# Kernel tuning notes

Measured on AMD Instinct MI355X. Metric: run time of the kernel, lower is better.

The kernel has to match this reference:

```python
import jax, jax.numpy as jnp
import numpy as np

J = 17
MIN_TORSO_H = 10.0
MAX_RANGE = 5.0
EPS = 1e-6
LN_EPS = 1e-5
LS, RS, LH, RH = 5, 6, 11, 12  # COCO shoulder/hip indices


def _mid(pl, pr, cl, cr):
    # conf-weighted midpoint: both valid -> mean, one valid -> that one, none -> 0
    wl = (cl > 0).astype(pl.dtype)[:, None]
    wr = (cr > 0).astype(pr.dtype)[:, None]
    s = wl * pl + wr * pr
    w = wl + wr
    return s / jnp.maximum(w, 1.0)


def torso_centric(kp):
    pos = kp[..., :2]          # [B, J, 2]
    conf = kp[..., 2:3]        # [B, J, 1]
    sc = conf[:, [LS, RS], 0]  # [B, 2]
    hc = conf[:, [LH, RH], 0]
    use_torso = ((sc > 0).sum(1) >= 1) & ((hc > 0).sum(1) >= 1)  # [B]
    sm = _mid(pos[:, LS], pos[:, RS], sc[:, 0], sc[:, 1])  # [B, 2]
    hm = _mid(pos[:, LH], pos[:, RH], hc[:, 0], hc[:, 1])
    sm = jnp.where(use_torso[:, None], sm, 0.0)
    hm = jnp.where(use_torso[:, None], hm, 0.0)
    center = (sm + hm) * 0.5                                   # [B, 2]
    height = jnp.linalg.norm(sm - hm, axis=1, keepdims=True)   # [B, 1]
    valid = use_torso & (height[:, 0] >= MIN_TORSO_H)
    torso_np = jnp.clip((pos - center[:, None, :]) / (height[:, None, :] + EPS),
                        -MAX_RANGE, MAX_RANGE)
    # bbox fallback (bbox computed from keypoints)
    mn = pos.min(axis=1, keepdims=True)
    mx = pos.max(axis=1, keepdims=True)
    bbox_np = jnp.clip((pos - mn) / (mx - mn + EPS), -MAX_RANGE, MAX_RANGE)
    norm_pos = jnp.where(valid[:, None, None], torso_np, bbox_np)
    return jnp.concatenate([norm_pos, conf], axis=-1)


def _ln(x, g, b):
    m = x.mean(-1, keepdims=True)
    v = ((x - m) ** 2).mean(-1, keepdims=True)
    return (x - m) / jnp.sqrt(v + LN_EPS) * g + b


def setup_inputs() -> dict:
    key = jax.random.key(0)
    ks = jax.random.split(key, 24)
    B = 32768

    def mk_kp(k0, k1, k2):
        pos = jax.random.uniform(k0, (B, J, 2)) * 512.0
        conf = jax.random.uniform(k1, (B, J, 1))
        conf = jnp.where(jax.random.uniform(k2, (B, J, 1)) < 0.2, 0.0, conf)
        return jnp.concatenate([pos, conf], -1)

    inp = {
        'keypoints': mk_kp(ks[0], ks[1], ks[2]),
        'prev_keypoints': mk_kp(ks[3], ks[4], ks[5]),
        'joint_emb': jax.random.normal(ks[6], (J, 16)) * 0.05,
        'pos_W': jax.random.normal(ks[7], (2, 16)) * 0.05, 'pos_b': jnp.zeros((16,)),
        'vel_W': jax.random.normal(ks[8], (2, 8)) * 0.05, 'vel_b': jnp.zeros((8,)),
        'angvel_W': jax.random.normal(ks[9], (3, 8)) * 0.05, 'angvel_b': jnp.zeros((8,)),
        'rel_W': jax.random.normal(ks[10], (2, 8)) * 0.05, 'rel_b': jnp.zeros((8,)),
        'conf_W': jax.random.normal(ks[11], (1, 4)) * 0.05, 'conf_b': jnp.zeros((4,)),
        'p1_W': jax.random.normal(ks[12], (60, 128)) * 0.05, 'p1_b': jnp.zeros((128,)),
        'ln1_g': jnp.ones((128,)), 'ln1_b': jnp.zeros((128,)),
        'p2_W': jax.random.normal(ks[13], (128, 64)) * 0.05, 'p2_b': jnp.zeros((64,)),
        'ln2_g': jnp.ones((64,)), 'ln2_b': jnp.zeros((64,)),
    }
    return inp


def reference(keypoints, prev_keypoints, joint_emb,
              pos_W, pos_b, vel_W, vel_b, angvel_W, angvel_b,
              rel_W, rel_b, conf_W, conf_b,
              p1_W, p1_b, ln1_g, ln1_b, p2_W, p2_b, ln2_g, ln2_b):
    B = keypoints.shape[0]
    kp = torso_centric(keypoints)
    pkp = torso_centric(prev_keypoints)
    pos = kp[..., :2]
    conf = kp[..., 2:3]

    type_emb = jnp.broadcast_to(joint_emb[None], (B, J, 16))
    pos_emb = pos @ pos_W + pos_b                               # [B,J,16]
    vel = pos - pkp[..., :2]
    vel_emb = vel @ vel_W + vel_b                               # [B,J,8]
    # use_angles=False -> angular velocities are zeros through the encoder
    angvel_emb = jnp.broadcast_to(angvel_b[None, None], (B, J, 8))
    # relative position to torso center (mean of shoulder/hip joints)
    torso_center = pos[:, jnp.array([LS, RS, LH, RH])].mean(axis=1, keepdims=True)
    rel_emb = (pos - torso_center) @ rel_W + rel_b              # [B,J,8]
    conf_emb = conf @ conf_W + conf_b                           # [B,J,4]

    feats = jnp.concatenate([type_emb, pos_emb, vel_emb, angvel_emb,
                             rel_emb, conf_emb], axis=-1)       # [B,J,60]
    h = _ln(feats @ p1_W + p1_b, ln1_g, ln1_b)
    h = jax.nn.relu(h)                                          # dropout is identity (eval)
    out = _ln(h @ p2_W + p2_b, ln2_g, ln2_b)                    # [B,J,64]
    return out
```

## Files before the change

kernel.cpp:

```cpp
#include <hip/hip_runtime.h>
#include <hip/hip_bf16.h>

#define NJ 17
#define ROWS 32
#define TPB 256
#define TOKPB (ROWS * NJ)

#define LSJ 5
#define RSJ 6
#define LHJ 11
#define RHJ 12

#define WSU_A1   4096
#define WSU_PRM  6144

#define SH_G1P  4096
#define SH_B1P  4160
#define SH_LN2  4224
#define SH_U32  4416

typedef __attribute__((ext_vector_type(8))) short bf16x8;
typedef __attribute__((ext_vector_type(8))) _Float16 f16x8;
typedef __attribute__((ext_vector_type(2))) _Float16 f16x2;
typedef __attribute__((ext_vector_type(4))) float f32x4;
typedef __attribute__((ext_vector_type(4))) unsigned int u32x4;

__device__ __forceinline__ unsigned short f2hu(float x) {
    _Float16 h = (_Float16)x;
    return __builtin_bit_cast(unsigned short, h);
}
__device__ __forceinline__ f16x2 cvt2h(float lo, float hi) {
    return __builtin_bit_cast(f16x2, __builtin_amdgcn_cvt_pkrtz(lo, hi));
}

__device__ __forceinline__ float row16_sum(float s) {
    int t;
    t = __builtin_amdgcn_update_dpp(0, __builtin_bit_cast(int, s), 0x121, 0xf, 0xf, true);
    s += __builtin_bit_cast(float, t);
    t = __builtin_amdgcn_update_dpp(0, __builtin_bit_cast(int, s), 0x122, 0xf, 0xf, true);
    s += __builtin_bit_cast(float, t);
    t = __builtin_amdgcn_update_dpp(0, __builtin_bit_cast(int, s), 0x124, 0xf, 0xf, true);
    s += __builtin_bit_cast(float, t);
    t = __builtin_amdgcn_update_dpp(0, __builtin_bit_cast(int, s), 0x128, 0xf, 0xf, true);
    s += __builtin_bit_cast(float, t);
    return s;
}

__device__ __forceinline__ void norm_row(const float* __restrict__ r,
                                         float* __restrict__ ox,
                                         float* __restrict__ oy) {
    float sc0 = r[LSJ*3+2], sc1 = r[RSJ*3+2];
    float hc0 = r[LHJ*3+2], hc1 = r[RHJ*3+2];
    bool ut = ((sc0 > 0.f) || (sc1 > 0.f)) && ((hc0 > 0.f) || (hc1 > 0.f));

    float wl = sc0 > 0.f ? 1.f : 0.f;
    float wr = sc1 > 0.f ? 1.f : 0.f;
    float ws = fmaxf(wl + wr, 1.f);
    float smx = (wl * r[LSJ*3+0] + wr * r[RSJ*3+0]) / ws;
    float smy = (wl * r[LSJ*3+1] + wr * r[RSJ*3+1]) / ws;

    wl = hc0 > 0.f ? 1.f : 0.f;
    wr = hc1 > 0.f ? 1.f : 0.f;
    ws = fmaxf(wl + wr, 1.f);
    float hmx = (wl * r[LHJ*3+0] + wr * r[RHJ*3+0]) / ws;
    float hmy = (wl * r[LHJ*3+1] + wr * r[RHJ*3+1]) / ws;

    if (!ut) { smx = 0.f; smy = 0.f; hmx = 0.f; hmy = 0.f; }

    float cx = (smx + hmx) * 0.5f;
    float cy = (smy + hmy) * 0.5f;
    float dx = smx - hmx, dy = smy - hmy;
    float hh = sqrtf(dx * dx + dy * dy);
    bool valid = ut && (hh >= 10.0f);

    float mnx = r[0], mxx = r[0], mny = r[1], mxy = r[1];
    #pragma unroll
    for (int j = 1; j < NJ; ++j) {
        float x = r[j*3], y = r[j*3+1];
        mnx = fminf(mnx, x); mxx = fmaxf(mxx, x);
        mny = fminf(mny, y); mxy = fmaxf(mxy, y);
    }

    float ih  = 1.f / (hh + 1e-6f);
    float ibx = 1.f / (mxx - mnx + 1e-6f);
    float iby = 1.f / (mxy - mny + 1e-6f);

    #pragma unroll
    for (int j = 0; j < NJ; ++j) {
        float x = r[j*3], y = r[j*3+1];
        float tx = (x - cx) * ih, ty = (y - cy) * ih;
        float bx = (x - mnx) * ibx, by = (y - mny) * iby;
        float nx = valid ? tx : bx;
        float ny = valid ? ty : by;
        ox[j] = fminf(fmaxf(nx, -5.f), 5.f);
        oy[j] = fminf(fmaxf(ny, -5.f), 5.f);
    }
}

__global__ __launch_bounds__(256) void setup_kernel(
    const float* __restrict__ emb,
    const float* __restrict__ posW, const float* __restrict__ posB,
    const float* __restrict__ velW, const float* __restrict__ velB,
    const float* __restrict__ angB,
    const float* __restrict__ relW, const float* __restrict__ relB,
    const float* __restrict__ confW, const float* __restrict__ confB,
    const float* __restrict__ P1, const float* __restrict__ p1b,
    const float* __restrict__ g1, const float* __restrict__ b1,
    const float* __restrict__ W2, const float* __restrict__ p2b,
    const float* __restrict__ g2, const float* __restrict__ b2,
    unsigned int* __restrict__ ws)
{
    __shared__ float sPA[7][128];
    __shared__ float sBase[128];
    __shared__ float sK0[17][128];
    const int tid = threadIdx.x;

    if (tid < 128) {
        const int n = tid;
        float pa0 = 0.f, pa1 = 0.f;
        #pragma unroll
        for (int i = 0; i < 16; ++i) {
            float w = P1[(16 + i) * 128 + n];
            pa0 += posW[i] * w; pa1 += posW[16 + i] * w;
        }
        float pv0 = 0.f, pv1 = 0.f;
        #pragma unroll
        for (int i = 0; i < 8; ++i) {
            float w = P1[(32 + i) * 128 + n];
            pv0 += velW[i] * w; pv1 += velW[8 + i] * w;
        }
        float pr0 = 0.f, pr1 = 0.f;
        #pragma unroll
        for (int i = 0; i < 8; ++i) {
            float w = P1[(48 + i) * 128 + n];
            pr0 += relW[i] * w; pr1 += relW[8 + i] * w;
        }
        float pc = 0.f;
        #pragma unroll
        for (int i = 0; i < 4; ++i) pc += confW[i] * P1[(56 + i) * 128 + n];

        float base = p1b[n];
        #pragma unroll
        for (int i = 0; i < 16; ++i) base += posB[i]  * P1[(16 + i) * 128 + n];
        #pragma unroll
        for (int i = 0; i < 8; ++i)  base += velB[i]  * P1[(32 + i) * 128 + n];
        #pragma unroll
        for (int i = 0; i < 8; ++i)  base += angB[i]  * P1[(40 + i) * 128 + n];
        #pragma unroll
        for (int i = 0; i < 8; ++i)  base += relB[i]  * P1[(48 + i) * 128 + n];
        #pragma unroll
        for (int i = 0; i < 4; ++i)  base += confB[i] * P1[(56 + i) * 128 + n];

        sPA[0][n] = pa0; sPA[1][n] = pa1;
        sPA[2][n] = pv0; sPA[3][n] = pv1;
        sPA[4][n] = pr0; sPA[5][n] = pr1;
        sPA[6][n] = pc;  sBase[n] = base;
    } else {
        const int t = tid - 128;
        const int n = t & 63;
        const int gp = (t >> 6) * 2;
        const unsigned xm = (unsigned)(n & 15) << 4;
        #pragma unroll
        for (int dg = 0; dg < 2; ++dg) {
            const int gg = gp + dg;
            #pragma unroll
            for (int ks = 0; ks < 4; ++ks) {
                unsigned int pk[4];
                #pragma unroll
                for (int ep = 0; ep < 4; ++ep) {
                    int e0 = 2 * ep, e1 = 2 * ep + 1;
                    int c0 = 4 * gg + (e0 & 3) + 16 * (2 * ks + (e0 >> 2));
                    int c1 = 4 * gg + (e1 & 3) + 16 * (2 * ks + (e1 >> 2));
                    unsigned lo = f2hu(W2[c0 * 64 + n]);
                    unsigned hi = f2hu(W2[c1 * 64 + n]);
                    pk[ep] = lo | (hi << 16);
                }
                unsigned byte = (unsigned)n * 256u + ((unsigned)((ks * 4 + gg) * 16) ^ xm);
                *(u32x4*)&ws[byte >> 2] = (u32x4){pk[0], pk[1], pk[2], pk[3]};
            }
        }
    }

    if (tid < 32) {
        const int gg = tid >> 3, nt1 = tid & 7;
        const int c0 = 4 * gg + 16 * nt1;
        ws[WSU_PRM + tid * 2 + 0]      = (unsigned)f2hu(g1[c0+0]) | ((unsigned)f2hu(g1[c0+1]) << 16);
        ws[WSU_PRM + tid * 2 + 1]      = (unsigned)f2hu(g1[c0+2]) | ((unsigned)f2hu(g1[c0+3]) << 16);
        ws[WSU_PRM + 64 + tid * 2 + 0] = (unsigned)f2hu(b1[c0+0]) | ((unsigned)f2hu(b1[c0+1]) << 16);
        ws[WSU_PRM + 64 + tid * 2 + 1] = (unsigned)f2hu(b1[c0+2]) | ((unsigned)f2hu(b1[c0+3]) << 16);
    } else if (tid >= 64 && tid < 256) {
        const int i = tid - 64;
        float v = (i < 64) ? g2[i] : (i < 128 ? b2[i - 64] : p2b[i - 128]);
        ws[WSU_PRM + 128 + i] = __builtin_bit_cast(unsigned, v);
    }
    __syncthreads();

    for (int e = tid; e < NJ * 128; e += 256) {
        int j = e >> 7, n = e & 127;
        float v = sBase[n];
        #pragma unroll
        for (int t = 0; t < 16; ++t) v += emb[j * 16 + t] * P1[t * 128 + n];
        sK0[j][n] = v;
    }
    __syncthreads();

    for (int i = tid; i < 512; i += 256) {
        const int nt1 = i >> 6, ln = i & 63, gg = ln >> 4, tl2 = ln & 15;
        const int ch = tl2 + 16 * nt1;
        float w[8];
        #pragma unroll
        for (int e = 0; e < 8; ++e) w[e] = 0.f;
        if (gg == 0) {
            #pragma unroll
            for (int e = 0; e < 7; ++e) w[e] = sPA[e][ch];
            w[7] = sK0[0][ch];
        } else if (gg == 1) {
            #pragma unroll
            for (int e = 0; e < 8; ++e) w[e] = sK0[e + 1][ch];
        } else if (gg == 2) {
            #pragma unroll
            for (int e = 0; e < 8; ++e) w[e] = sK0[e + 9][ch];
        }
        unsigned u[4];
        #pragma unroll
        for (int p = 0; p < 4; ++p) {
            unsigned short lo = f2hu(w[2*p]);
            unsigned short hi = f2hu(w[2*p+1]);
            u[p] = (unsigned)lo | ((unsigned)hi << 16);
        }
        *(u32x4*)&ws[WSU_A1 + i * 4] = (u32x4){u[0], u[1], u[2], u[3]};
    }
}

__global__ __launch_bounds__(TPB, 2)
void jfe_kernel(
    const float* __restrict__ kp, const float* __restrict__ pkp,
    const unsigned int* __restrict__ ws,
    float* __restrict__ out, int B)
{
    __shared__ __align__(16) unsigned int sWS[SH_U32];
    __shared__ __align__(16) unsigned int sA1[2176];
    __shared__ __align__(16) float4 sPk[TOKPB];
    __shared__ __align__(8)  float2 sQ[TOKPB];
    __shared__ float2 sTc[ROWS];

    const int tid  = threadIdx.x;
    const int lane = tid & 63;
    const int wv   = tid >> 6;
    const int g    = lane >> 4;
    const int tl   = lane & 15;

    const int row0  = blockIdx.x * ROWS;
    const int nrows = min(ROWS, B - row0);
    const long long tok0 = (long long)blockIdx.x * TOKPB;
    const long long ntok = (long long)B * NJ;

    for (int c = tid; c < 1024; c += TPB)
        *(u32x4*)&sWS[c * 4] = *(const u32x4*)&ws[c * 4];
    for (int c = tid; c < 512; c += TPB)
        *(u32x4*)&sA1[c * 4] = *(const u32x4*)&ws[WSU_A1 + c * 4];
    if (tid < 80)
        *(u32x4*)&sWS[SH_G1P + tid * 4] = *(const u32x4*)&ws[WSU_PRM + tid * 4];

    if (tl < 16 && g == 0) {
        const int task  = wv * 16 + tl;
        const int frame = task >> 5;
        const int row   = task & 31;
        if (row < nrows) {
            float ox[NJ], oy[NJ];
            if (frame == 0) {
                const float* rp = kp + (long long)(row0 + row) * 51;
                norm_row(rp, ox, oy);
                #pragma unroll
                for (int j = 0; j < NJ; ++j)
                    sPk[row * NJ + j] = make_float4(ox[j], oy[j], rp[j * 3 + 2], 0.f);
                sTc[row] = make_float2(
                    0.25f * (ox[LSJ] + ox[RSJ] + ox[LHJ] + ox[RHJ]),
                    0.25f * (oy[LSJ] + oy[RSJ] + oy[LHJ] + oy[RHJ]));
            } else {
                norm_row(pkp + (long long)(row0 + row) * 51, ox, oy);
                #pragma unroll
                for (int j = 0; j < NJ; ++j)
                    sQ[row * NJ + j] = make_float2(ox[j], oy[j]);
            }
        }
    }
    __syncthreads();

    f16x8 a1f[8];
    #pragma unroll
    for (int nt1 = 0; nt1 < 8; ++nt1)
        a1f[nt1] = __builtin_bit_cast(f16x8,
            *(const u32x4*)&sA1[(nt1 * 64 + lane) * 4]);

    f16x2 g1h[8][2], b1h[8][2];
    #pragma unroll
    for (int nt1 = 0; nt1 < 8; ++nt1) {
        g1h[nt1][0] = __builtin_bit_cast(f16x2, sWS[SH_G1P + (g * 8 + nt1) * 2 + 0]);
        g1h[nt1][1] = __builtin_bit_cast(f16x2, sWS[SH_G1P + (g * 8 + nt1) * 2 + 1]);
        b1h[nt1][0] = __builtin_bit_cast(f16x2, sWS[SH_B1P + (g * 8 + nt1) * 2 + 0]);
        b1h[nt1][1] = __builtin_bit_cast(f16x2, sWS[SH_B1P + (g * 8 + nt1) * 2 + 1]);
    }
    float g2v[4], b2v[4], p2v[4];
    #pragma unroll
    for (int nt = 0; nt < 4; ++nt) {
        g2v[nt] = __builtin_bit_cast(float, sWS[SH_LN2 +   0 + 4 * tl + nt]);
        b2v[nt] = __builtin_bit_cast(float, sWS[SH_LN2 +  64 + 4 * tl + nt]);
        p2v[nt] = __builtin_bit_cast(float, sWS[SH_LN2 + 128 + nt * 16 + tl]);
    }
    __syncthreads();

    float* const sXp = (float*)sA1 + wv * 544 + g * 136;

    const bool full = (nrows == ROWS);
    const int ntiles = (nrows * NJ + 15) >> 4;
    const unsigned xm = (unsigned)tl << 4;

    #pragma unroll 1
    for (int t = wv; t < ntiles; t += 4) {
        const int tbase = t * 16;
        const int tok = tbase + tl;
        const int r = (tok * 3856) >> 16;
        const int j = tok - r * NJ;

        const float4 pk = sPk[tok];
        const float2 qv = sQ[tok];
        const float2 tc = sTc[r];
        const float px = pk.x, py = pk.y, cf = pk.z;
        const float vx = px - qv.x, vy = py - qv.y;
        const float rx = px - tc.x, ry = py - tc.y;

        f16x8 bf;
        {
            const int base7 = g * 8 - 7;
            #pragma unroll
            for (int e = 0; e < 8; ++e) {
                float oh = ((base7 + e) == j) ? 1.f : 0.f;
                float val;
                if (e == 0) val = (g == 0) ? px : oh;
                else if (e == 1) val = (g == 0) ? py : oh;
                else if (e == 2) val = (g == 0) ? vx : oh;
                else if (e == 3) val = (g == 0) ? vy : oh;
                else if (e == 4) val = (g == 0) ? rx : oh;
                else if (e == 5) val = (g == 0) ? ry : oh;
                else if (e == 6) val = (g == 0) ? cf : oh;
                else val = oh;
                bf[e] = (_Float16)val;
            }
        }

        f32x4 acc1[8];
        #pragma unroll
        for (int nt1 = 0; nt1 < 8; ++nt1)
            acc1[nt1] = __builtin_amdgcn_mfma_f32_16x16x32_f16(
                a1f[nt1], bf, (f32x4){0.f, 0.f, 0.f, 0.f}, 0, 0, 0);

        float s, ss;
        {
            float t0[8], t1[8];
            #pragma unroll
            for (int n1 = 0; n1 < 8; ++n1) {
                float a0 = acc1[n1][0], a1 = acc1[n1][1];
                float a2 = acc1[n1][2], a3 = acc1[n1][3];
                t0[n1] = (a0 + a1) + (a2 + a3);
                t1[n1] = (a0 * a0 + a1 * a1) + (a2 * a2 + a3 * a3);
            }
            s  = ((t0[0] + t0[1]) + (t0[2] + t0[3])) + ((t0[4] + t0[5]) + (t0[6] + t0[7]));
            ss = ((t1[0] + t1[1]) + (t1[2] + t1[3])) + ((t1[4] + t1[5]) + (t1[6] + t1[7]));
        }
        s += __shfl_xor(s, 16); ss += __shfl_xor(ss, 16);
        s += __shfl_xor(s, 32); ss += __shfl_xor(ss, 32);
        const float mu  = s * (1.f / 128.f);
        const float inv = rsqrtf(ss * (1.f / 128.f) - mu * mu + 1e-5f);

        const f16x2 im2 = cvt2h(inv, inv);
        const f16x2 nm2 = cvt2h(-mu * inv, -mu * inv);
        const f16x2 zero2 = (f16x2)(_Float16)0.f;
        u32x4 afu[4];
        #pragma unroll
        for (int nt1 = 0; nt1 < 8; ++nt1) {
            const int ks = nt1 >> 1, sl = 2 * (nt1 & 1);
            f16x2 a01 = cvt2h(acc1[nt1][0], acc1[nt1][1]);
            f16x2 a23 = cvt2h(acc1[nt1][2], acc1[nt1][3]);
            f16x2 s01 = g1h[nt1][0] * im2;
            f16x2 s23 = g1h[nt1][1] * im2;
            f16x2 c01 = g1h[nt1][0] * nm2 + b1h[nt1][0];
            f16x2 c23 = g1h[nt1][1] * nm2 + b1h[nt1][1];
            f16x2 t01 = __builtin_elementwise_max(a01 * s01 + c01, zero2);
            f16x2 t23 = __builtin_elementwise_max(a23 * s23 + c23, zero2);
            afu[ks][sl + 0] = __builtin_bit_cast(unsigned, t01);
            afu[ks][sl + 1] = __builtin_bit_cast(unsigned, t23);
        }

        f32x4 acc2[4];
        #pragma unroll
        for (int nt = 0; nt < 4; ++nt)
            acc2[nt] = (f32x4){p2v[nt], p2v[nt], p2v[nt], p2v[nt]};
        #pragma unroll
        for (int ks = 0; ks < 4; ++ks) {
            const unsigned so = ((unsigned)((ks * 4 + g) * 16) ^ xm) >> 2;
            const f16x8 afk = __builtin_bit_cast(f16x8, afu[ks]);
            #pragma unroll
            for (int nt = 0; nt < 4; ++nt) {
                const unsigned idx = (unsigned)(nt * 16 + tl) * 64u + so;
                f16x8 bw = __builtin_bit_cast(f16x8, *(const u32x4*)&sWS[idx]);
                acc2[nt] = __builtin_amdgcn_mfma_f32_16x16x32_f16(afk, bw, acc2[nt], 0, 0, 0);
            }
        }

        float vm[4], vi[4];
        #pragma unroll
        for (int q = 0; q < 4; ++q) {
            float a0 = acc2[0][q], a1 = acc2[1][q], a2 = acc2[2][q], a3 = acc2[3][q];
            float s2 = row16_sum((a0 + a1) + (a2 + a3));
            float q2 = row16_sum((a0 * a0 + a1 * a1) + (a2 * a2 + a3 * a3));
            vm[q] = s2 * (1.f / 64.f);
            vi[q] = rsqrtf(q2 * (1.f / 64.f) - vm[q] * vm[q] + 1e-5f);
        }
        float* const obase = out + (((long long)(tok0 + tbase) + g * 4) << 6) + 4 * tl;

#define WRQ(q, rr) { \
        float* d = sXp + (rr) * 68; \
        d[ 0 + tl] = (acc2[0][q] - vm[q]) * vi[q]; \
        d[16 + tl] = (acc2[1][q] - vm[q]) * vi[q]; \
        d[32 + tl] = (acc2[2][q] - vm[q]) * vi[q]; \
        d[48 + tl] = (acc2[3][q] - vm[q]) * vi[q]; }
#define RDQ(q, rr) { \
        f32x4 w = *(const f32x4*)&sXp[(rr) * 68 + 4 * tl]; \
        f32x4 v; \
        v[0] = w[0] * g2v[0] + b2v[0]; v[1] = w[1] * g2v[1] + b2v[1]; \
        v[2] = w[2] * g2v[2] + b2v[2]; v[3] = w[3] * g2v[3] + b2v[3]; \
        *(f32x4*)(obase + (q) * 64) = v; }
#define RDQG(q, rr) { \
        if (tok0 + tbase + g * 4 + (q) < ntok) RDQ(q, rr) }

        if (full) {
            WRQ(0, 0); WRQ(1, 1); RDQ(0, 0);
            WRQ(2, 0); RDQ(1, 1);
            WRQ(3, 1); RDQ(2, 0); RDQ(3, 1);
        } else {
            WRQ(0, 0); WRQ(1, 1); RDQG(0, 0);
            WRQ(2, 0); RDQG(1, 1);
            WRQ(3, 1); RDQG(2, 0); RDQG(3, 1);
        }
#undef WRQ
#undef RDQ
#undef RDQG
    }
}

extern "C" void kernel_launch(void* const* d_in, const int* in_sizes, int n_in,
                              void* d_out, int out_size, void* d_ws, size_t ws_size,
                              hipStream_t stream) {
    const float* kp    = (const float*)d_in[0];
    const float* pkp   = (const float*)d_in[1];
    const float* emb   = (const float*)d_in[2];
    const float* posW  = (const float*)d_in[3];
    const float* posB  = (const float*)d_in[4];
    const float* velW  = (const float*)d_in[5];
    const float* velB  = (const float*)d_in[6];
    const float* angB  = (const float*)d_in[8];
    const float* relW  = (const float*)d_in[9];
    const float* relB  = (const float*)d_in[10];
    const float* confW = (const float*)d_in[11];
    const float* confB = (const float*)d_in[12];
    const float* P1    = (const float*)d_in[13];
    const float* p1b   = (const float*)d_in[14];
    const float* g1    = (const float*)d_in[15];
    const float* b1    = (const float*)d_in[16];
    const float* W2    = (const float*)d_in[17];
    const float* p2b   = (const float*)d_in[18];
    const float* g2    = (const float*)d_in[19];
    const float* b2    = (const float*)d_in[20];
    float* out = (float*)d_out;
    unsigned int* ws = (unsigned int*)d_ws;

    int B = in_sizes[0] / (NJ * 3);

    setup_kernel<<<1, 256, 0, stream>>>(
        emb, posW, posB, velW, velB, angB, relW, relB, confW, confB,
        P1, p1b, g1, b1, W2, p2b, g2, b2, ws);

    int nblocks = (B + ROWS - 1) / ROWS;
    jfe_kernel<<<nblocks, TPB, 0, stream>>>(kp, pkp, ws, out, B);
}
```

Baseline: 59.61 us.

## Software-pipeline tile loop: issue next tile's first GEMM before current epilogue

Splits the per-tile body into a front stage (input gather plus first MFMA layer) and a back stage (LayerNorm, second MFMA, output). The loop is restructured with double-buffered accumulators so the next tile's first-layer MFMAs are issued before the current tile's back stage, letting matrix work overlap with the ALU, shuffle and store work. It also folds the final LN subtraction into an FMA. Holding two sets of accumulators raises register pressure under a 2-waves launch bound, which may cause spills. The first front_tile runs unguarded even when a wave has no tile.

```diff
diff --git a/kernel.cpp b/kernel.cpp
--- a/kernel.cpp
+++ b/kernel.cpp
@@ -230,6 +230,148 @@
         }
         *(u32x4*)&ws[WSU_A1 + i * 4] = (u32x4){u[0], u[1], u[2], u[3]};
     }
+}
+
+__device__ __forceinline__ void front_tile(
+    const int tbase, const int tl, const int g,
+    const float4* __restrict__ sPk, const float2* __restrict__ sQ,
+    const float2* __restrict__ sTc,
+    const f16x8 (&a1f)[8], f32x4 (&acc1)[8])
+{
+    const int tok = tbase + tl;
+    const int r = (tok * 3856) >> 16;
+    const int j = tok - r * NJ;
+
+    const float4 pk = sPk[tok];
+    const float2 qv = sQ[tok];
+    const float2 tc = sTc[r];
+    const float px = pk.x, py = pk.y, cf = pk.z;
+    const float vx = px - qv.x, vy = py - qv.y;
+    const float rx = px - tc.x, ry = py - tc.y;
+
+    f16x8 bf;
+    const int base7 = g * 8 - 7;
+    #pragma unroll
+    for (int e = 0; e < 8; ++e) {
+        float oh = ((base7 + e) == j) ? 1.f : 0.f;
+        float val;
+        if (e == 0) val = (g == 0) ? px : oh;
+        else if (e == 1) val = (g == 0) ? py : oh;
+        else if (e == 2) val = (g == 0) ? vx : oh;
+        else if (e == 3) val = (g == 0) ? vy : oh;
+        else if (e == 4) val = (g == 0) ? rx : oh;
+        else if (e == 5) val = (g == 0) ? ry : oh;
+        else if (e == 6) val = (g == 0) ? cf : oh;
+        else val = oh;
+        bf[e] = (_Float16)val;
+    }
+
+    #pragma unroll
+    for (int nt1 = 0; nt1 < 8; ++nt1)
+        acc1[nt1] = __builtin_amdgcn_mfma_f32_16x16x32_f16(
+            a1f[nt1], bf, (f32x4){0.f, 0.f, 0.f, 0.f}, 0, 0, 0);
+}
+
+__device__ __forceinline__ void back_tile(
+    const int tbase, const int tl, const int g, const unsigned xm,
+    const long long tok0, const long long ntok, const bool full,
+    const unsigned int* __restrict__ sWS, float* __restrict__ sXp,
+    const f16x2 (&g1h)[8][2], const f16x2 (&b1h)[8][2],
+    const float (&g2v)[4], const float (&b2v)[4], const float (&p2v)[4],
+    const f32x4 (&acc1)[8], float* __restrict__ out)
+{
+    float s, ss;
+    {
+        float t0[8], t1[8];
+        #pragma unroll
+        for (int n1 = 0; n1 < 8; ++n1) {
+            float a0 = acc1[n1][0], a1 = acc1[n1][1];
+            float a2 = acc1[n1][2], a3 = acc1[n1][3];
+            t0[n1] = (a0 + a1) + (a2 + a3);
+            t1[n1] = (a0 * a0 + a1 * a1) + (a2 * a2 + a3 * a3);
+        }
+        s  = ((t0[0] + t0[1]) + (t0[2] + t0[3])) + ((t0[4] + t0[5]) + (t0[6] + t0[7]));
+        ss = ((t1[0] + t1[1]) + (t1[2] + t1[3])) + ((t1[4] + t1[5]) + (t1[6] + t1[7]));
+    }
+    s += __shfl_xor(s, 16); ss += __shfl_xor(ss, 16);
+    s += __shfl_xor(s, 32); ss += __shfl_xor(ss, 32);
+    const float mu  = s * (1.f / 128.f);
+    const float inv = rsqrtf(ss * (1.f / 128.f) - mu * mu + 1e-5f);
+
+    const f16x2 im2 = cvt2h(inv, inv);
+    const f16x2 nm2 = cvt2h(-mu * inv, -mu * inv);
+    const f16x2 zero2 = (f16x2)(_Float16)0.f;
+    u32x4 afu[4];
+    #pragma unroll
+    for (int nt1 = 0; nt1 < 8; ++nt1) {
+        const int ks = nt1 >> 1, sl = 2 * (nt1 & 1);
+        f16x2 a01 = cvt2h(acc1[nt1][0], acc1[nt1][1]);
+        f16x2 a23 = cvt2h(acc1[nt1][2], acc1[nt1][3]);
+        f16x2 s01 = g1h[nt1][0] * im2;
+        f16x2 s23 = g1h[nt1][1] * im2;
+        f16x2 c01 = g1h[nt1][0] * nm2 + b1h[nt1][0];
+        f16x2 c23 = g1h[nt1][1] * nm2 + b1h[nt1][1];
+        f16x2 t01 = __builtin_elementwise_max(a01 * s01 + c01, zero2);
+        f16x2 t23 = __builtin_elementwise_max(a23 * s23 + c23, zero2);
+        afu[ks][sl + 0] = __builtin_bit_cast(unsigned, t01);
+        afu[ks][sl + 1] = __builtin_bit_cast(unsigned, t23);
+    }
+
+    f32x4 acc2[4];
+    #pragma unroll
+    for (int nt = 0; nt < 4; ++nt)
+        acc2[nt] = (f32x4){p2v[nt], p2v[nt], p2v[nt], p2v[nt]};
+    #pragma unroll
+    for (int ks = 0; ks < 4; ++ks) {
+        const unsigned so = ((unsigned)((ks * 4 + g) * 16) ^ xm) >> 2;
+        const f16x8 afk = __builtin_bit_cast(f16x8, afu[ks]);
+        #pragma unroll
+        for (int nt = 0; nt < 4; ++nt) {
+            const unsigned idx = (unsigned)(nt * 16 + tl) * 64u + so;
+            f16x8 bw = __builtin_bit_cast(f16x8, *(const u32x4*)&sWS[idx]);
+            acc2[nt] = __builtin_amdgcn_mfma_f32_16x16x32_f16(afk, bw, acc2[nt], 0, 0, 0);
+        }
+    }
+
+    float vi[4], nvi[4];
+    #pragma unroll
+    for (int q = 0; q < 4; ++q) {
+        float a0 = acc2[0][q], a1 = acc2[1][q], a2 = acc2[2][q], a3 = acc2[3][q];
+        float s2 = row16_sum((a0 + a1) + (a2 + a3));
+        float q2 = row16_sum((a0 * a0 + a1 * a1) + (a2 * a2 + a3 * a3));
+        float m = s2 * (1.f / 64.f);
+        vi[q]  = rsqrtf(q2 * (1.f / 64.f) - m * m + 1e-5f);
+        nvi[q] = -m * vi[q];
+    }
+    float* const obase = out + (((long long)(tok0 + tbase) + g * 4) << 6) + 4 * tl;
+
+#define WRQ(q, rr) { \
+    float* d = sXp + (rr) * 68; \
+    d[ 0 + tl] = acc2[0][q] * vi[q] + nvi[q]; \
+    d[16 + tl] = acc2[1][q] * vi[q] + nvi[q]; \
+    d[32 + tl] = acc2[2][q] * vi[q] + nvi[q]; \
+    d[48 + tl] = acc2[3][q] * vi[q] + nvi[q]; }
+#define RDQ(q, rr) { \
+    f32x4 w = *(const f32x4*)&sXp[(rr) * 68 + 4 * tl]; \
+    f32x4 v; \
+    v[0] = w[0] * g2v[0] + b2v[0]; v[1] = w[1] * g2v[1] + b2v[1]; \
+    v[2] = w[2] * g2v[2] + b2v[2]; v[3] = w[3] * g2v[3] + b2v[3]; \
+    *(f32x4*)(obase + (q) * 64) = v; }
+#define RDQG(q, rr) { \
+    if (tok0 + tbase + g * 4 + (q) < ntok) RDQ(q, rr) }
+
+    if (full) {
+        WRQ(0, 0); WRQ(1, 1); RDQ(0, 0);
+        WRQ(2, 0); RDQ(1, 1);
+        WRQ(3, 1); RDQ(2, 0); RDQ(3, 1);
+    } else {
+        WRQ(0, 0); WRQ(1, 1); RDQG(0, 0);
+        WRQ(2, 0); RDQG(1, 1);
+        WRQ(3, 1); RDQG(2, 0); RDQG(3, 1);
+    }
+#undef WRQ
+#undef RDQ
+#undef RDQG
 }
 
 __global__ __launch_bounds__(TPB, 2)
@@ -316,136 +458,23 @@
     const int ntiles = (nrows * NJ + 15) >> 4;
     const unsigned xm = (unsigned)tl << 4;
 
-    #pragma unroll 1
-    for (int t = wv; t < ntiles; t += 4) {
-        const int tbase = t * 16;
-        const int tok = tbase + tl;
-        const int r = (tok * 3856) >> 16;
-        const int j = tok - r * NJ;
-
-        const float4 pk = sPk[tok];
-        const float2 qv = sQ[tok];
-        const float2 tc = sTc[r];
-        const float px = pk.x, py = pk.y, cf = pk.z;
-        const float vx = px - qv.x, vy = py - qv.y;
-        const float rx = px - tc.x, ry = py - tc.y;
-
-        f16x8 bf;
-        {
-            const int base7 = g * 8 - 7;
-            #pragma unroll
-            for (int e = 0; e < 8; ++e) {
-                float oh = ((base7 + e) == j) ? 1.f : 0.f;
-                float val;
-                if (e == 0) val = (g == 0) ? px : oh;
-                else if (e == 1) val = (g == 0) ? py : oh;
-                else if (e == 2) val = (g == 0) ? vx : oh;
-                else if (e == 3) val = (g == 0) ? vy : oh;
-                else if (e == 4) val = (g == 0) ? rx : oh;
-                else if (e == 5) val = (g == 0) ? ry : oh;
-                else if (e == 6) val = (g == 0) ? cf : oh;
-                else val = oh;
-                bf[e] = (_Float16)val;
-            }
-        }
-
-        f32x4 acc1[8];
-        #pragma unroll
-        for (int nt1 = 0; nt1 < 8; ++nt1)
-            acc1[nt1] = __builtin_amdgcn_mfma_f32_16x16x32_f16(
-                a1f[nt1], bf, (f32x4){0.f, 0.f, 0.f, 0.f}, 0, 0, 0);
-
-        float s, ss;
-        {
-            float t0[8], t1[8];
-            #pragma unroll
-            for (int n1 = 0; n1 < 8; ++n1) {
-                float a0 = acc1[n1][0], a1 = acc1[n1][1];
-                float a2 = acc1[n1][2], a3 = acc1[n1][3];
-                t0[n1] = (a0 + a1) + (a2 + a3);
-                t1[n1] = (a0 * a0 + a1 * a1) + (a2 * a2 + a3 * a3);
-            }
-            s  = ((t0[0] + t0[1]) + (t0[2] + t0[3])) + ((t0[4] + t0[5]) + (t0[6] + t0[7]));
-            ss = ((t1[0] + t1[1]) + (t1[2] + t1[3])) + ((t1[4] + t1[5]) + (t1[6] + t1[7]));
-        }
-        s += __shfl_xor(s, 16); ss += __shfl_xor(ss, 16);
-        s += __shfl_xor(s, 32); ss += __shfl_xor(ss, 32);
-        const float mu  = s * (1.f / 128.f);
-        const float inv = rsqrtf(ss * (1.f / 128.f) - mu * mu + 1e-5f);
-
-        const f16x2 im2 = cvt2h(inv, inv);
-        const f16x2 nm2 = cvt2h(-mu * inv, -mu * inv);
-        const f16x2 zero2 = (f16x2)(_Float16)0.f;
-        u32x4 afu[4];
-        #pragma unroll
-        for (int nt1 = 0; nt1 < 8; ++nt1) {
-            const int ks = nt1 >> 1, sl = 2 * (nt1 & 1);
-            f16x2 a01 = cvt2h(acc1[nt1][0], acc1[nt1][1]);
-            f16x2 a23 = cvt2h(acc1[nt1][2], acc1[nt1][3]);
-            f16x2 s01 = g1h[nt1][0] * im2;
-            f16x2 s23 = g1h[nt1][1] * im2;
-            f16x2 c01 = g1h[nt1][0] * nm2 + b1h[nt1][0];
-            f16x2 c23 = g1h[nt1][1] * nm2 + b1h[nt1][1];
-            f16x2 t01 = __builtin_elementwise_max(a01 * s01 + c01, zero2);
-            f16x2 t23 = __builtin_elementwise_max(a23 * s23 + c23, zero2);
-            afu[ks][sl + 0] = __builtin_bit_cast(unsigned, t01);
-            afu[ks][sl + 1] = __builtin_bit_cast(unsigned, t23);
-        }
-
-        f32x4 acc2[4];
-        #pragma unroll
-        for (int nt = 0; nt < 4; ++nt)
-            acc2[nt] = (f32x4){p2v[nt], p2v[nt], p2v[nt], p2v[nt]};
-        #pragma unroll
-        for (int ks = 0; ks < 4; ++ks) {
-            const unsigned so = ((unsigned)((ks * 4 + g) * 16) ^ xm) >> 2;
-            const f16x8 afk = __builtin_bit_cast(f16x8, afu[ks]);
-            #pragma unroll
-            for (int nt = 0; nt < 4; ++nt) {
-                const unsigned idx = (unsigned)(nt * 16 + tl) * 64u + so;
-                f16x8 bw = __builtin_bit_cast(f16x8, *(const u32x4*)&sWS[idx]);
-                acc2[nt] = __builtin_amdgcn_mfma_f32_16x16x32_f16(afk, bw, acc2[nt], 0, 0, 0);
-            }
-        }
-
-        float vm[4], vi[4];
-        #pragma unroll
-        for (int q = 0; q < 4; ++q) {
-            float a0 = acc2[0][q], a1 = acc2[1][q], a2 = acc2[2][q], a3 = acc2[3][q];
-            float s2 = row16_sum((a0 + a1) + (a2 + a3));
-            float q2 = row16_sum((a0 * a0 + a1 * a1) + (a2 * a2 + a3 * a3));
-            vm[q] = s2 * (1.f / 64.f);
-            vi[q] = rsqrtf(q2 * (1.f / 64.f) - vm[q] * vm[q] + 1e-5f);
-        }
-        float* const obase = out + (((long long)(tok0 + tbase) + g * 4) << 6) + 4 * tl;
-
-#define WRQ(q, rr) { \
-        float* d = sXp + (rr) * 68; \
-        d[ 0 + tl] = (acc2[0][q] - vm[q]) * vi[q]; \
-        d[16 + tl] = (acc2[1][q] - vm[q]) * vi[q]; \
-        d[32 + tl] = (acc2[2][q] - vm[q]) * vi[q]; \
-        d[48 + tl] = (acc2[3][q] - vm[q]) * vi[q]; }
-#define RDQ(q, rr) { \
-        f32x4 w = *(const f32x4*)&sXp[(rr) * 68 + 4 * tl]; \
-        f32x4 v; \
-        v[0] = w[0] * g2v[0] + b2v[0]; v[1] = w[1] * g2v[1] + b2v[1]; \
-        v[2] = w[2] * g2v[2] + b2v[2]; v[3] = w[3] * g2v[3] + b2v[3]; \
-        *(f32x4*)(obase + (q) * 64) = v; }
-#define RDQG(q, rr) { \
-        if (tok0 + tbase + g * 4 + (q) < ntok) RDQ(q, rr) }
-
-        if (full) {
-            WRQ(0, 0); WRQ(1, 1); RDQ(0, 0);
-            WRQ(2, 0); RDQ(1, 1);
-            WRQ(3, 1); RDQ(2, 0); RDQ(3, 1);
-        } else {
-            WRQ(0, 0); WRQ(1, 1); RDQG(0, 0);
-            WRQ(2, 0); RDQG(1, 1);
-            WRQ(3, 1); RDQG(2, 0); RDQG(3, 1);
-        }
-#undef WRQ
-#undef RDQ
-#undef RDQG
+    f32x4 accA[8], accB[8];
+    int t = wv;
+    front_tile(t * 16, tl, g, sPk, sQ, sTc, a1f, accA);
+    while (true) {
+        if (t + 4 < ntiles)
+            front_tile((t + 4) * 16, tl, g, sPk, sQ, sTc, a1f, accB);
+        back_tile(t * 16, tl, g, xm, tok0, ntok, full, sWS, sXp,
+                  g1h, b1h, g2v, b2v, p2v, accA, out);
+        t += 4;
+        if (t >= ntiles) break;
+
+        if (t + 4 < ntiles)
+            front_tile((t + 4) * 16, tl, g, sPk, sQ, sTc, a1f, accA);
+        back_tile(t * 16, tl, g, xm, tok0, ntok, full, sWS, sXp,
+                  g1h, b1h, g2v, b2v, p2v, accB, out);
+        t += 4;
+        if (t >= ntiles) break;
     }
 }
 
```

Result: slower. 117.3 us (+96.8%).
